# Kernel optimization log

Hardware: AMD Instinct MI355X
Metric: run time of the kernel (lower is better)

The kernel has to match this reference:

```python
import jax, jax.numpy as jnp
import numpy as np

B, T, C = 2, 2048, 1024
E, F = 8, 1024        # n_experts, expert ffn dim
FS = 2048             # shared expert ffn dim
TOP_K = 2


def setup_inputs() -> dict:
    key = jax.random.key(0)
    ks = jax.random.split(key, 6)
    s = lambda *d: 1.0 / np.sqrt(d[-1])
    return {
        "hidden_tensor": jax.random.normal(ks[0], (B, T, C), jnp.float32),
        "w_router": jax.random.normal(ks[1], (E, C), jnp.float32) * s(C),
        "w1_stack": jax.random.normal(ks[2], (E, F, C), jnp.float32) * s(C),
        "w2_stack": jax.random.normal(ks[3], (E, C, F), jnp.float32) * s(F),
        "ws1": jax.random.normal(ks[4], (FS, C), jnp.float32) * s(C),
        "ws2": jax.random.normal(ks[5], (C, FS), jnp.float32) * s(FS),
    }


def reference(hidden_tensor, w_router, w1_stack, w2_stack, ws1, ws2):
    Bb, Tt, Cc = hidden_tensor.shape
    x = hidden_tensor.reshape(-1, Cc)                      # (t, C)
    t = x.shape[0]

    # --- router: softmax over experts, top-k, renormalize ---
    logits = x @ w_router.T                                # (t, E)
    probs = jax.nn.softmax(logits, axis=-1)
    expert_weight, expert_idx = jax.lax.top_k(probs, TOP_K)  # (t, k)
    expert_weight = expert_weight / jnp.sum(expert_weight, axis=-1, keepdims=True)

    # --- dispatch: stable sort token-expert pairs by expert id ---
    flat_e = expert_idx.reshape(-1)                        # (t*k,)
    order = jnp.argsort(flat_e, stable=True)
    sorted_e = flat_e[order]
    flat_tok = jnp.repeat(jnp.arange(t), TOP_K)
    sorted_tok = flat_tok[order]
    sorted_w = expert_weight.reshape(-1)[order]

    counts = jnp.bincount(sorted_e, length=E)              # (E,)
    offsets = jnp.concatenate([jnp.zeros((1,), counts.dtype), jnp.cumsum(counts)])
    local_pos = jnp.arange(t * TOP_K) - offsets[sorted_e]  # position within expert bin

    cap = t * TOP_K  # static capacity (>= true cnt_max), padding rows stay zero
    binned = jnp.zeros((E, cap, Cc), x.dtype).at[sorted_e, local_pos].set(x[sorted_tok])

    # --- grouped expert FFN with squared-ReLU ---
    inter = jnp.einsum('ecd,efd->ecf', binned, w1_stack)   # (E, cap, F)
    inter = jnp.square(jax.nn.relu(inter))
    outb = jnp.einsum('ecf,edf->ecd', inter, w2_stack)     # (E, cap, C)

    # --- combine: gather back, weight, scatter-add to tokens ---
    flat_out = outb[sorted_e, local_pos] * sorted_w[:, None]
    moe_out = jnp.zeros((t, Cc), x.dtype).at[sorted_tok].add(flat_out)
    moe_out = moe_out.reshape(Bb, Tt, Cc)

    # --- shared expert on residual (squared-ReLU MLP) ---
    sh = jnp.square(jax.nn.relu(jnp.einsum('btc,fc->btf', hidden_tensor, ws1)))
    shared_out = jnp.einsum('btf,cf->btc', sh, ws2)

    return shared_out + moe_out
```

## Files before the change

### kernel.cpp

```cpp
#include <hip/hip_runtime.h>
#include <math.h>

typedef unsigned short u16;
typedef unsigned int u32;

typedef __attribute__((ext_vector_type(8))) short bf16x8;
typedef __attribute__((ext_vector_type(4))) float f32x4;

__device__ __forceinline__ u16 f2bf(float f) {
  union { float f; u32 u; } v; v.f = f;
  u32 r = v.u + 0x7FFFu + ((v.u >> 16) & 1u);
  return (u16)(r >> 16);
}

typedef const u32 __attribute__((address_space(1)))* gas1_t;
typedef u32 __attribute__((address_space(3)))* las3_t;

__device__ __forceinline__ void gload16(const void* g, void* l) {
  __builtin_amdgcn_global_load_lds((gas1_t)g, (las3_t)l, 16, 0, 0);
}

struct Tile { int kind; int g0; int n0; int e; };

__global__ __launch_bounds__(256) void convert_weights(
    const float4* __restrict__ w1, const float4* __restrict__ w2,
    const float4* __restrict__ s1, const float4* __restrict__ s2,
    ushort4* __restrict__ o1, ushort4* __restrict__ o2,
    ushort4* __restrict__ o3, ushort4* __restrict__ o4) {
  size_t i = (size_t)blockIdx.x * 256 + threadIdx.x;
  const size_t n1 = 2097152, n2 = 2097152, n3 = 524288;
  float4 v; ushort4* o; size_t j;
  if (i < n1)              { v = w1[i];            o = o1; j = i; }
  else if (i < n1+n2)      { v = w2[i-n1];         o = o2; j = i-n1; }
  else if (i < n1+n2+n3)   { v = s1[i-n1-n2];      o = o3; j = i-n1-n2; }
  else                     { v = s2[i-n1-n2-n3];   o = o4; j = i-n1-n2-n3; }
  ushort4 r; r.x = f2bf(v.x); r.y = f2bf(v.y); r.z = f2bf(v.z); r.w = f2bf(v.w);
  o[j] = r;
}

__global__ __launch_bounds__(256) void router_kernel(
    const float* __restrict__ x, const float* __restrict__ wr,
    u16* __restrict__ xb, int* __restrict__ tokE, float* __restrict__ tokW) {
  const int wv = threadIdx.x >> 6, lane = threadIdx.x & 63;
  const int tok = blockIdx.x * 4 + wv;
  const float4* xp = (const float4*)(x + (size_t)tok * 1024);
  float4 xv[4];
#pragma unroll
  for (int i = 0; i < 4; ++i) xv[i] = xp[i * 64 + lane];
  ushort4* xo = (ushort4*)xb + (size_t)tok * 256;
#pragma unroll
  for (int i = 0; i < 4; ++i) {
    ushort4 o;
    o.x = f2bf(xv[i].x); o.y = f2bf(xv[i].y); o.z = f2bf(xv[i].z); o.w = f2bf(xv[i].w);
    xo[i * 64 + lane] = o;
  }
  float acc[8];
#pragma unroll
  for (int e = 0; e < 8; ++e) acc[e] = 0.f;
#pragma unroll
  for (int e = 0; e < 8; ++e) {
    const float4* wp = (const float4*)(wr + e * 1024);
#pragma unroll
    for (int i = 0; i < 4; ++i) {
      float4 w4 = wp[i * 64 + lane];
      acc[e] += xv[i].x * w4.x + xv[i].y * w4.y + xv[i].z * w4.z + xv[i].w * w4.w;
    }
  }
#pragma unroll
  for (int m = 32; m > 0; m >>= 1)
#pragma unroll
    for (int e = 0; e < 8; ++e) acc[e] += __shfl_xor(acc[e], m, 64);
  if (lane == 0) {
    int e0 = 0;
#pragma unroll
    for (int e = 1; e < 8; ++e) if (acc[e] > acc[e0]) e0 = e;
    int e1 = (e0 == 0) ? 1 : 0;
#pragma unroll
    for (int e = 0; e < 8; ++e) if (e != e0 && acc[e] > acc[e1]) e1 = e;
    float p1 = __expf(acc[e1] - acc[e0]);
    float w1 = p1 / (1.f + p1);
    float w0 = 1.f - w1;
    tokE[tok * 2] = e0; tokE[tok * 2 + 1] = e1;
    tokW[tok * 2] = w0; tokW[tok * 2 + 1] = w1;
  }
}

__global__ __launch_bounds__(256) void plan_kernel(
    const int* __restrict__ tokE, const float* __restrict__ tokW,
    Tile* __restrict__ upT, Tile* __restrict__ downT,
    int* __restrict__ rowtok, float* __restrict__ roww, int* __restrict__ invrow) {
  const int t = threadIdx.x, lane = t & 63, wv = t >> 6;
  int myE[32];
#pragma unroll
  for (int i = 0; i < 32; ++i) myE[i] = tokE[t * 32 + i];
  int lcnt[8] = {};
#pragma unroll
  for (int i = 0; i < 32; ++i) ++lcnt[myE[i]];

  __shared__ int wtot[8][4];
  __shared__ int aoffS[9];
  __shared__ int etile[72 * 2];
  int excl[8];
#pragma unroll
  for (int e = 0; e < 8; ++e) {
    int v = lcnt[e];
#pragma unroll
    for (int off = 1; off < 64; off <<= 1) {
      int n = __shfl_up(v, (unsigned)off, 64);
      if (lane >= off) v += n;
    }
    if (lane == 63) wtot[e][wv] = v;
    excl[e] = v - lcnt[e];
  }
  __syncthreads();
#pragma unroll
  for (int e = 0; e < 8; ++e)
    for (int w = 0; w < wv; ++w) excl[e] += wtot[e][w];

  if (t == 0) {
    int s = 0, ti = 0;
    for (int e = 0; e < 8; ++e) {
      aoffS[e] = s;
      int cnt = wtot[e][0] + wtot[e][1] + wtot[e][2] + wtot[e][3];
      int tiles = (cnt + 127) >> 7;
      for (int k = 0; k < tiles; ++k) { etile[2 * ti] = e; etile[2 * ti + 1] = s + k * 128; ++ti; }
      s += tiles << 7;
    }
    aoffS[8] = s;
    for (; ti < 72; ++ti) { etile[2 * ti] = -1; etile[2 * ti + 1] = 0; }
  }
  for (int i = t; i < 9216; i += 256) { rowtok[i] = 0; roww[i] = 0.f; }
  __syncthreads();

  for (int i = t; i < 1088; i += 256) {
    Tile tl;
    if (i < 512) { tl.kind = 0; tl.g0 = (i >> 4) * 128; tl.n0 = (i & 15) * 128; tl.e = 0; }
    else {
      int j = i - 512, mi = j >> 3, n = j & 7;
      int e = etile[2 * mi];
      tl.kind = (e < 0) ? -1 : 1; tl.g0 = etile[2 * mi + 1]; tl.n0 = n * 128; tl.e = (e < 0) ? 0 : e;
    }
    upT[i] = tl;
  }
  for (int i = t; i < 832; i += 256) {
    Tile tl;
    if (i < 256) { tl.kind = 0; tl.g0 = (i >> 3) * 128; tl.n0 = (i & 7) * 128; tl.e = 0; }
    else {
      int j = i - 256, mi = j >> 3, n = j & 7;
      int e = etile[2 * mi];
      tl.kind = (e < 0) ? -1 : 1; tl.g0 = etile[2 * mi + 1]; tl.n0 = n * 128; tl.e = (e < 0) ? 0 : e;
    }
    downT[i] = tl;
  }

  int pos[8];
#pragma unroll
  for (int e = 0; e < 8; ++e) pos[e] = aoffS[e] + excl[e];
#pragma unroll
  for (int i = 0; i < 32; ++i) {
    int idx = t * 32 + i;
    int e = myE[i];
    int g = pos[e]++;
    rowtok[g] = idx >> 1;
    roww[g] = tokW[idx];
    invrow[idx] = g;
  }
}

__global__ __launch_bounds__(256) void combine_kernel(
    const float* __restrict__ Ym, const int* __restrict__ invrow,
    const float* __restrict__ tokW, float* __restrict__ out) {
  const int t = blockIdx.x;
  const int r0 = invrow[2 * t], r1 = invrow[2 * t + 1];
  const float w0 = tokW[2 * t], w1 = tokW[2 * t + 1];
  const float4* y0 = (const float4*)(Ym + (size_t)r0 * 1024);
  const float4* y1 = (const float4*)(Ym + (size_t)r1 * 1024);
  float4* o = (float4*)(out + (size_t)t * 1024);
  const int c = threadIdx.x;
  float4 a = y0[c], b = y1[c], v = o[c];
  v.x += w0 * a.x + w1 * b.x;
  v.y += w0 * a.y + w1 * b.y;
  v.z += w0 * a.z + w1 * b.z;
  v.w += w0 * a.w + w1 * b.w;
  o[c] = v;
}

template <int PHASE>
__global__ __launch_bounds__(256)
void gemm_fused(const Tile* __restrict__ tiles,
                const u16* __restrict__ A0, const u16* __restrict__ B0, void* __restrict__ C0,
                const u16* __restrict__ A1, const u16* __restrict__ B1, void* __restrict__ C1,
                const int* __restrict__ rowtok, const float* __restrict__ roww) {
  __shared__ u16 As[128 * 32];
  __shared__ u16 Bs[128 * 32];

  Tile tm = tiles[blockIdx.x];
  if (tm.kind < 0) return;
  if (PHASE == 2 && tm.kind != 0) return;
  if (PHASE == 3 && tm.kind != 1) return;

  const int tid = threadIdx.x;
  const int lane = tid & 63;
  const int wv = tid >> 6;
  const int wrow = wv >> 1, wcol = wv & 1;

  const u16* A; const u16* B; void* C; int N, K;
  if (tm.kind == 0) {
    A = A0; B = B0; C = C0;
    N = (PHASE == 0) ? 2048 : 1024;
    K = (PHASE == 0) ? 1024 : 2048;
  } else {
    A = A1; B = B1 + ((size_t)tm.e << 20); C = (PHASE == 3) ? C0 : C1;
    N = 1024; K = 1024;
  }
  const int g0 = tm.g0, n0 = tm.n0;

  const u16* aSrc[2];
  const u16* bSrc[2];
  u32 ldsOff[2];
#pragma unroll
  for (int p = 0; p < 2; ++p) {
    int c = p * 256 + tid;
    int row = c >> 2;
    int q = ((c & 3) - (c >> 3)) & 3;
    int arow = g0 + row;
    if (PHASE == 0 && tm.kind == 1) arow = rowtok[arow];
    aSrc[p] = A + (size_t)arow * K + q * 8;
    bSrc[p] = B + (size_t)(n0 + row) * K + q * 8;
    ldsOff[p] = (u32)(p * 256 + wv * 64) * 16u;
  }

  const int fr = lane & 15, fq = lane >> 4;
  const int sw = ((fq + (fr >> 1)) & 3) * 8;
  const int aRd = (wrow * 64 + fr) * 32 + sw;
  const int bRd = (wcol * 64 + fr) * 32 + sw;

  f32x4 acc[4][4] = {};

  for (int k0 = 0; k0 < K; k0 += 32) {
#pragma unroll
    for (int p = 0; p < 2; ++p) {
      gload16(aSrc[p] + k0, (char*)As + ldsOff[p]);
      gload16(bSrc[p] + k0, (char*)Bs + ldsOff[p]);
    }
    __syncthreads();
    bf16x8 af[4], bfg[4];
#pragma unroll
    for (int i = 0; i < 4; ++i) af[i] = *(const bf16x8*)&As[aRd + i * 512];
#pragma unroll
    for (int j = 0; j < 4; ++j) bfg[j] = *(const bf16x8*)&Bs[bRd + j * 512];
#pragma unroll
    for (int i = 0; i < 4; ++i)
#pragma unroll
      for (int j = 0; j < 4; ++j)
        acc[i][j] = __builtin_amdgcn_mfma_f32_16x16x32_bf16(af[i], bfg[j], acc[i][j], 0, 0, 0);
    __syncthreads();
  }

  if (PHASE == 0) {
    u16* O = (u16*)C;
#pragma unroll
    for (int i = 0; i < 4; ++i) {
      int rb = g0 + wrow * 64 + i * 16 + fq * 4;
#pragma unroll
      for (int j = 0; j < 4; ++j) {
        int col = n0 + wcol * 64 + j * 16 + fr;
#pragma unroll
        for (int r = 0; r < 4; ++r) {
          float v = acc[i][j][r];
          v = v > 0.f ? v * v : 0.f;
          O[(size_t)(rb + r) * N + col] = f2bf(v);
        }
      }
    }
  } else if (PHASE == 1 || PHASE == 2) {
    float* O = (float*)C;
#pragma unroll
    for (int i = 0; i < 4; ++i) {
      int rb = g0 + wrow * 64 + i * 16 + fq * 4;
#pragma unroll
      for (int j = 0; j < 4; ++j) {
        int col = n0 + wcol * 64 + j * 16 + fr;
#pragma unroll
        for (int r = 0; r < 4; ++r)
          O[(size_t)(rb + r) * N + col] = acc[i][j][r];
      }
    }
  } else {
    float* O = (float*)C;
#pragma unroll
    for (int i = 0; i < 4; ++i) {
      int rb = g0 + wrow * 64 + i * 16 + fq * 4;
#pragma unroll
      for (int r = 0; r < 4; ++r) {
        int tok = rowtok[rb + r];
        float w = roww[rb + r];
#pragma unroll
        for (int j = 0; j < 4; ++j) {
          int col = n0 + wcol * 64 + j * 16 + fr;
          atomicAdd(&O[(size_t)tok * N + col], w * acc[i][j][r]);
        }
      }
    }
  }
}

extern "C" void kernel_launch(void* const* d_in, const int* in_sizes, int n_in,
                              void* d_out, int out_size, void* d_ws, size_t ws_size,
                              hipStream_t stream) {
  const float* x   = (const float*)d_in[0];
  const float* wr  = (const float*)d_in[1];
  const float* w1  = (const float*)d_in[2];
  const float* w2  = (const float*)d_in[3];
  const float* s1  = (const float*)d_in[4];
  const float* s2  = (const float*)d_in[5];
  float* out = (float*)d_out;

  char* p = (char*)d_ws;
  auto alloc = [&](size_t n) { char* r = p; p += (n + 255) & ~(size_t)255; return r; };
  u16* xb   = (u16*)alloc(4096ULL * 1024 * 2);
  u16* w1b  = (u16*)alloc(8ULL * 1024 * 1024 * 2);
  u16* w2b  = (u16*)alloc(8ULL * 1024 * 1024 * 2);
  u16* s1b  = (u16*)alloc(2048ULL * 1024 * 2);
  u16* s2b  = (u16*)alloc(1024ULL * 2048 * 2);
  u16* Hs   = (u16*)alloc(4096ULL * 2048 * 2);
  u16* Hm   = (u16*)alloc(9216ULL * 1024 * 2);
  int* tokE = (int*)alloc(8192 * 4);
  float* tokW = (float*)alloc(8192 * 4);
  int* rowtok = (int*)alloc(9216 * 4);
  float* roww = (float*)alloc(9216 * 4);
  int* invrow = (int*)alloc(8192 * 4);
  Tile* upT   = (Tile*)alloc(1088 * sizeof(Tile));
  Tile* downT = (Tile*)alloc(832 * sizeof(Tile));
  size_t used_base = (size_t)(p - (char*)d_ws);
  float* Ym = (float*)p;
  const bool haveYm = (ws_size - used_base) >= 9216ULL * 1024 * 4;

  convert_weights<<<20480, 256, 0, stream>>>(
      (const float4*)w1, (const float4*)w2, (const float4*)s1, (const float4*)s2,
      (ushort4*)w1b, (ushort4*)w2b, (ushort4*)s1b, (ushort4*)s2b);

  router_kernel<<<1024, 256, 0, stream>>>(x, wr, xb, tokE, tokW);
  plan_kernel<<<1, 256, 0, stream>>>(tokE, tokW, upT, downT, rowtok, roww, invrow);

  gemm_fused<0><<<1088, 256, 0, stream>>>(upT, xb, s1b, Hs, xb, w1b, Hm, rowtok, roww);

  if (haveYm) {
    gemm_fused<1><<<832, 256, 0, stream>>>(downT, Hs, s2b, out, Hm, w2b, Ym, rowtok, roww);
    combine_kernel<<<4096, 256, 0, stream>>>(Ym, invrow, tokW, out);
  } else {
    gemm_fused<2><<<832, 256, 0, stream>>>(downT, Hs, s2b, out, Hm, w2b, nullptr, rowtok, roww);
    gemm_fused<3><<<832, 256, 0, stream>>>(downT, Hs, s2b, out, Hm, w2b, nullptr, rowtok, roww);
  }
}
```

Baseline: 290.3 us.

## Double GEMM K-tile, group tile order for L2 reuse, store expert output as bf16

The GEMM main loop now stages 64-wide K slices in LDS with a new 8-slot swizzle, which halves the number of barrier pairs per tile. The up and down tile lists are reordered into grouped blocks so that concurrently running workgroups share A and B panels in L2. The expert down-projection intermediate is written as bf16 instead of fp32, cutting write and combine read traffic. The trade-offs are extra rounding error on the expert outputs and doubled LDS use per block, which may lower occupancy.

```diff
diff --git a/kernel.cpp b/kernel.cpp
--- a/kernel.cpp
+++ b/kernel.cpp
@@ -11,6 +11,9 @@
   union { float f; u32 u; } v; v.f = f;
   u32 r = v.u + 0x7FFFu + ((v.u >> 16) & 1u);
   return (u16)(r >> 16);
+}
+__device__ __forceinline__ float bf2f(u16 h) {
+  union { u32 u; float f; } v; v.u = ((u32)h) << 16; return v.f;
 }
 
 typedef const u32 __attribute__((address_space(1)))* gas1_t;
@@ -133,22 +136,38 @@
   __syncthreads();
 
   for (int i = t; i < 1088; i += 256) {
+    int x = i & 7, s = i >> 3;
     Tile tl;
-    if (i < 512) { tl.kind = 0; tl.g0 = (i >> 4) * 128; tl.n0 = (i & 15) * 128; tl.e = 0; }
-    else {
-      int j = i - 512, mi = j >> 3, n = j & 7;
+    if (s < 64) {
+      int gg = x & 3, nn = x >> 2;
+      int gl = s & 7, nl = s >> 3;
+      tl.kind = 0; tl.g0 = (gg * 8 + gl) * 128; tl.n0 = (nn * 8 + nl) * 128; tl.e = 0;
+    } else {
+      int s2_ = s - 64;
+      int mg = x & 3, ng = x >> 2;
+      int ml = s2_ % 18, nl = s2_ / 18;
+      int mi = mg * 18 + ml;
       int e = etile[2 * mi];
-      tl.kind = (e < 0) ? -1 : 1; tl.g0 = etile[2 * mi + 1]; tl.n0 = n * 128; tl.e = (e < 0) ? 0 : e;
+      tl.kind = (e < 0) ? -1 : 1; tl.g0 = etile[2 * mi + 1];
+      tl.n0 = (ng * 4 + nl) * 128; tl.e = (e < 0) ? 0 : e;
     }
     upT[i] = tl;
   }
   for (int i = t; i < 832; i += 256) {
+    int x = i & 7, s = i >> 3;
     Tile tl;
-    if (i < 256) { tl.kind = 0; tl.g0 = (i >> 3) * 128; tl.n0 = (i & 7) * 128; tl.e = 0; }
-    else {
-      int j = i - 256, mi = j >> 3, n = j & 7;
+    if (s < 32) {
+      int gg = x & 3, nn = x >> 2;
+      int gl = s & 7, nl = s >> 3;
+      tl.kind = 0; tl.g0 = (gg * 8 + gl) * 128; tl.n0 = (nn * 4 + nl) * 128; tl.e = 0;
+    } else {
+      int s2_ = s - 32;
+      int mg = x & 3, ng = x >> 2;
+      int ml = s2_ % 18, nl = s2_ / 18;
+      int mi = mg * 18 + ml;
       int e = etile[2 * mi];
-      tl.kind = (e < 0) ? -1 : 1; tl.g0 = etile[2 * mi + 1]; tl.n0 = n * 128; tl.e = (e < 0) ? 0 : e;
+      tl.kind = (e < 0) ? -1 : 1; tl.g0 = etile[2 * mi + 1];
+      tl.n0 = (ng * 4 + nl) * 128; tl.e = (e < 0) ? 0 : e;
     }
     downT[i] = tl;
   }
@@ -168,20 +187,21 @@
 }
 
 __global__ __launch_bounds__(256) void combine_kernel(
-    const float* __restrict__ Ym, const int* __restrict__ invrow,
+    const u16* __restrict__ Ym, const int* __restrict__ invrow,
     const float* __restrict__ tokW, float* __restrict__ out) {
   const int t = blockIdx.x;
   const int r0 = invrow[2 * t], r1 = invrow[2 * t + 1];
   const float w0 = tokW[2 * t], w1 = tokW[2 * t + 1];
-  const float4* y0 = (const float4*)(Ym + (size_t)r0 * 1024);
-  const float4* y1 = (const float4*)(Ym + (size_t)r1 * 1024);
+  const ushort4* y0 = (const ushort4*)(Ym + (size_t)r0 * 1024);
+  const ushort4* y1 = (const ushort4*)(Ym + (size_t)r1 * 1024);
   float4* o = (float4*)(out + (size_t)t * 1024);
   const int c = threadIdx.x;
-  float4 a = y0[c], b = y1[c], v = o[c];
-  v.x += w0 * a.x + w1 * b.x;
-  v.y += w0 * a.y + w1 * b.y;
-  v.z += w0 * a.z + w1 * b.z;
-  v.w += w0 * a.w + w1 * b.w;
+  ushort4 a = y0[c], b = y1[c];
+  float4 v = o[c];
+  v.x += w0 * bf2f(a.x) + w1 * bf2f(b.x);
+  v.y += w0 * bf2f(a.y) + w1 * bf2f(b.y);
+  v.z += w0 * bf2f(a.z) + w1 * bf2f(b.z);
+  v.w += w0 * bf2f(a.w) + w1 * bf2f(b.w);
   o[c] = v;
 }
 
@@ -191,8 +211,8 @@
                 const u16* __restrict__ A0, const u16* __restrict__ B0, void* __restrict__ C0,
                 const u16* __restrict__ A1, const u16* __restrict__ B1, void* __restrict__ C1,
                 const int* __restrict__ rowtok, const float* __restrict__ roww) {
-  __shared__ u16 As[128 * 32];
-  __shared__ u16 Bs[128 * 32];
+  __shared__ u16 As[128 * 64];
+  __shared__ u16 Bs[128 * 64];
 
   Tile tm = tiles[blockIdx.x];
   if (tm.kind < 0) return;
@@ -215,14 +235,14 @@
   }
   const int g0 = tm.g0, n0 = tm.n0;
 
-  const u16* aSrc[2];
-  const u16* bSrc[2];
-  u32 ldsOff[2];
-#pragma unroll
-  for (int p = 0; p < 2; ++p) {
+  const u16* aSrc[4];
+  const u16* bSrc[4];
+  u32 ldsOff[4];
+#pragma unroll
+  for (int p = 0; p < 4; ++p) {
     int c = p * 256 + tid;
-    int row = c >> 2;
-    int q = ((c & 3) - (c >> 3)) & 3;
+    int row = c >> 3, slot = c & 7;
+    int q = (slot - (row >> 1) - 4 * (row & 1)) & 7;
     int arow = g0 + row;
     if (PHASE == 0 && tm.kind == 1) arow = rowtok[arow];
     aSrc[p] = A + (size_t)arow * K + q * 8;
@@ -231,29 +251,35 @@
   }
 
   const int fr = lane & 15, fq = lane >> 4;
-  const int sw = ((fq + (fr >> 1)) & 3) * 8;
-  const int aRd = (wrow * 64 + fr) * 32 + sw;
-  const int bRd = (wcol * 64 + fr) * 32 + sw;
+  const int swBase = (fr >> 1) + 4 * (fr & 1);
+  const int sw0 = ((fq + swBase) & 7) * 8;
+  const int sw1 = ((fq + 4 + swBase) & 7) * 8;
+  const int aRow = (wrow * 64 + fr) * 64;
+  const int bRow = (wcol * 64 + fr) * 64;
 
   f32x4 acc[4][4] = {};
 
-  for (int k0 = 0; k0 < K; k0 += 32) {
-#pragma unroll
-    for (int p = 0; p < 2; ++p) {
+  for (int k0 = 0; k0 < K; k0 += 64) {
+#pragma unroll
+    for (int p = 0; p < 4; ++p) {
       gload16(aSrc[p] + k0, (char*)As + ldsOff[p]);
       gload16(bSrc[p] + k0, (char*)Bs + ldsOff[p]);
     }
     __syncthreads();
-    bf16x8 af[4], bfg[4];
-#pragma unroll
-    for (int i = 0; i < 4; ++i) af[i] = *(const bf16x8*)&As[aRd + i * 512];
-#pragma unroll
-    for (int j = 0; j < 4; ++j) bfg[j] = *(const bf16x8*)&Bs[bRd + j * 512];
-#pragma unroll
-    for (int i = 0; i < 4; ++i)
-#pragma unroll
-      for (int j = 0; j < 4; ++j)
-        acc[i][j] = __builtin_amdgcn_mfma_f32_16x16x32_bf16(af[i], bfg[j], acc[i][j], 0, 0, 0);
+#pragma unroll
+    for (int ks = 0; ks < 2; ++ks) {
+      const int sw = ks ? sw1 : sw0;
+      bf16x8 af[4], bfg[4];
+#pragma unroll
+      for (int i = 0; i < 4; ++i) af[i] = *(const bf16x8*)&As[aRow + i * 1024 + sw];
+#pragma unroll
+      for (int j = 0; j < 4; ++j) bfg[j] = *(const bf16x8*)&Bs[bRow + j * 1024 + sw];
+#pragma unroll
+      for (int i = 0; i < 4; ++i)
+#pragma unroll
+        for (int j = 0; j < 4; ++j)
+          acc[i][j] = __builtin_amdgcn_mfma_f32_16x16x32_bf16(af[i], bfg[j], acc[i][j], 0, 0, 0);
+    }
     __syncthreads();
   }
 
@@ -273,7 +299,35 @@
         }
       }
     }
-  } else if (PHASE == 1 || PHASE == 2) {
+  } else if (PHASE == 1) {
+    if (tm.kind == 0) {
+      float* O = (float*)C;
+#pragma unroll
+      for (int i = 0; i < 4; ++i) {
+        int rb = g0 + wrow * 64 + i * 16 + fq * 4;
+#pragma unroll
+        for (int j = 0; j < 4; ++j) {
+          int col = n0 + wcol * 64 + j * 16 + fr;
+#pragma unroll
+          for (int r = 0; r < 4; ++r)
+            O[(size_t)(rb + r) * N + col] = acc[i][j][r];
+        }
+      }
+    } else {
+      u16* O = (u16*)C;
+#pragma unroll
+      for (int i = 0; i < 4; ++i) {
+        int rb = g0 + wrow * 64 + i * 16 + fq * 4;
+#pragma unroll
+        for (int j = 0; j < 4; ++j) {
+          int col = n0 + wcol * 64 + j * 16 + fr;
+#pragma unroll
+          for (int r = 0; r < 4; ++r)
+            O[(size_t)(rb + r) * N + col] = f2bf(acc[i][j][r]);
+        }
+      }
+    }
+  } else if (PHASE == 2) {
     float* O = (float*)C;
 #pragma unroll
     for (int i = 0; i < 4; ++i) {
@@ -333,8 +387,8 @@
   Tile* upT   = (Tile*)alloc(1088 * sizeof(Tile));
   Tile* downT = (Tile*)alloc(832 * sizeof(Tile));
   size_t used_base = (size_t)(p - (char*)d_ws);
-  float* Ym = (float*)p;
-  const bool haveYm = (ws_size - used_base) >= 9216ULL * 1024 * 4;
+  u16* Ym = (u16*)p;
+  const bool haveYm = (ws_size - used_base) >= 9216ULL * 1024 * 2;
 
   convert_weights<<<20480, 256, 0, stream>>>(
       (const float4*)w1, (const float4*)w2, (const float4*)s1, (const float4*)s2,
```

Measured after the change: 289.2 us. Within noise of the previous version (-0.4%).
